# Kernel optimization log

Measured on AMD Instinct MI355X. Metric: run time of the kernel, lower is better.

Reference implementation:

```python
import jax, jax.numpy as jnp
import numpy as np

B, S, D_IN, E, H, WIN = 2, 4096, 512, 512, 8, 128
HD = E // H
NEG = -1e30


def setup_inputs() -> dict:
    key = jax.random.key(0)
    k0, k1, k2 = jax.random.split(key, 3)
    x = jax.random.normal(k0, (B, S, D_IN), jnp.float32)
    w_qkv = jax.random.normal(k1, (D_IN, 3 * E), jnp.float32) / np.sqrt(D_IN)
    b_qkv = jnp.zeros((3 * E,), jnp.float32)
    w_o = jax.random.normal(k2, (E, E), jnp.float32) / np.sqrt(E)
    b_o = jnp.zeros((E,), jnp.float32)
    return dict(x=x, w_qkv=w_qkv, b_qkv=b_qkv, w_o=w_o, b_o=b_o)


def _sliding_window_attn(q, k, v, w):
    # q,k,v: (B, S, H, HD). Longformer sliding-chunks: each query attends to
    # keys within +/- w positions (band of 2w+1), out-of-range masked to -inf.
    b, s, h, hd = q.shape
    assert s % (2 * w) == 0
    c = s // w  # number of width-w query chunks
    qc = q.transpose(0, 2, 1, 3).reshape(b, h, c, w, hd)  # (B,H,C,w,HD)

    def windows(t):
        # build per-chunk 3w key/value windows [c*w - w, c*w + 2w)
        t = t.transpose(0, 2, 1, 3)  # (B,H,S,HD)
        t = jnp.pad(t, ((0, 0), (0, 0), (w, w), (0, 0)))
        t = t.reshape(b, h, c + 2, w, hd)
        return jnp.concatenate([t[:, :, 0:c], t[:, :, 1:c + 1], t[:, :, 2:c + 2]], axis=3)  # (B,H,C,3w,HD)

    kc = windows(k)
    vc = windows(v)

    # chunked logits over the 3w window, scaled by sqrt(d_k)
    logits3 = jnp.einsum('bhcxd,bhcyd->bhcxy', qc, kc) / jnp.sqrt(jnp.asarray(hd, q.dtype))

    # extract diagonal band: band[x, r] = logits3[x, x + r], r in [0, 2w]
    row = jnp.arange(w)[:, None]            # (w,1)
    col = row + jnp.arange(2 * w + 1)[None, :]  # (w,2w+1), index into 3w window
    band = logits3[..., row, col]           # (B,H,C,w,2w+1)

    # mask positions outside [0, S): global key j = i + r - w
    i = (jnp.arange(c) * w)[:, None, None] + jnp.arange(w)[None, :, None]  # (C,w,1)
    j = i + (jnp.arange(2 * w + 1) - w)[None, None, :]                      # (C,w,2w+1)
    valid = (j >= 0) & (j < s)
    band = jnp.where(valid, band, NEG)

    probs = jax.nn.softmax(band, axis=-1)  # (B,H,C,w,2w+1)

    # scatter band probs back into the 3w window and contract with values
    probs3 = jnp.zeros_like(logits3).at[..., row, col].set(probs)  # (B,H,C,w,3w)
    out = jnp.einsum('bhcxy,bhcyd->bhcxd', probs3, vc)  # (B,H,C,w,HD)
    return out.reshape(b, h, s, hd).transpose(0, 2, 1, 3)  # (B,S,H,HD)


def reference(x, w_qkv, b_qkv, w_o, b_o):
    bsz, s, _ = x.shape
    qkv = x @ w_qkv + b_qkv                      # (B,S,3E)
    qkv = qkv.reshape(bsz, s, H, 3 * HD)
    q = qkv[..., :HD]
    k = qkv[..., HD:2 * HD]
    v = qkv[..., 2 * HD:]
    vals = _sliding_window_attn(q, k, v, WIN).reshape(bsz, s, E)
    return vals @ w_o + b_o
```

## Files before the change

kernel.cpp:

```cpp
#include <hip/hip_runtime.h>
#include <hip/hip_bf16.h>
#include <math.h>

typedef _Float16 f16;
typedef __attribute__((ext_vector_type(8))) _Float16 f16x8;
typedef __attribute__((ext_vector_type(4))) _Float16 f16x4;
typedef __attribute__((ext_vector_type(4))) float f32x4;

#define S_LEN 4096
#define NHEAD 8
#define HDIM 64
#define EMB 512
#define KDIM 512
#define LOG2E 1.4426950408889634f

#if __has_builtin(__builtin_amdgcn_exp2f)
#define EXP2F(x) __builtin_amdgcn_exp2f(x)
#else
#define EXP2F(x) exp2f(x)
#endif

__device__ __forceinline__ void g2l16(const void* g, void* l) {
  __builtin_amdgcn_global_load_lds(
      reinterpret_cast<const __attribute__((address_space(1))) unsigned int*>(
          reinterpret_cast<uintptr_t>(g)),
      reinterpret_cast<__attribute__((address_space(3))) unsigned int*>(
          static_cast<unsigned int>(reinterpret_cast<uintptr_t>(l))),
      16, 0, 0);
}

__global__ __launch_bounds__(256) void prep_kernel(
    const float* __restrict__ x, f16* __restrict__ xb,
    const float* __restrict__ w_qkv, f16* __restrict__ wqkvt,
    const float* __restrict__ w_o, f16* __restrict__ wot) {
  __shared__ f16 tile[64][65];
  const int bid = blockIdx.x;
  const int tid = threadIdx.x;
  if (bid < 4096) {
    const int i = (bid * 256 + tid) * 4;
    float4 v = *(const float4*)(x + i);
    f16x4 o = { (f16)v.x, (f16)v.y, (f16)v.z, (f16)v.w };
    *(f16x4*)(xb + i) = o;
    return;
  }
  const float* in;
  f16* out;
  int R, C, c0, r0;
  if (bid < 4288) {
    const int t = bid - 4096;
    in = w_qkv; out = wqkvt; R = 512; C = 1536;
    c0 = (t % 24) * 64; r0 = (t / 24) * 64;
  } else {
    const int t = bid - 4288;
    in = w_o; out = wot; R = 512; C = 512;
    c0 = (t & 7) * 64; r0 = (t >> 3) * 64;
  }
#pragma unroll
  for (int i = 0; i < 16; ++i) {
    const int idx = i * 256 + tid;
    const int lr = idx >> 6, lc = idx & 63;
    tile[lr][lc] = (f16)in[(size_t)(r0 + lr) * C + (c0 + lc)];
  }
  __syncthreads();
#pragma unroll
  for (int i = 0; i < 16; ++i) {
    const int idx = i * 256 + tid;
    const int lc = idx >> 6, lr = idx & 63;
    out[(size_t)(c0 + lc) * R + (r0 + lr)] = tile[lr][lc];
  }
}

#define TM 128
#define TK 32

template<int MODE, int TN>
__global__ __launch_bounds__(256) void gemm_bt_kernel(
    const f16* __restrict__ A, const f16* __restrict__ Bt, const float* __restrict__ bias,
    f16* __restrict__ Qo, f16* __restrict__ Ko, f16* __restrict__ Vo,
    float* __restrict__ Co, int M, int N) {
  constexpr int JN = TN / 32;
  constexpr int BCH = TN / 64;
  constexpr int SMEMSZ = (MODE == 0) ? (128 * 136 * 2) : (8192 + TN * TK * 2);
  __shared__ __align__(16) char smem[SMEMSZ];
  f16 (*As)[TK] = (f16 (*)[TK])smem;
  f16 (*Bs)[TK] = (f16 (*)[TK])(smem + 8192);
  const int m0 = blockIdx.x * TM, n0 = blockIdx.y * TN;
  const int tid = threadIdx.x;
  const int lane = tid & 63, wid = tid >> 6;
  const int wr = wid >> 1, wc = wid & 1;
  const int g = lane >> 4, q16 = lane & 15;

  const int srow = lane >> 2;
  const int skof = (lane & 3) * 8;
  const f16* Ag[2]; char* Al[2];
#pragma unroll
  for (int cb = 0; cb < 2; ++cb) {
    const int ch = wid * 2 + cb;
    Ag[cb] = A + (size_t)(m0 + ch * 16 + srow) * KDIM + skof;
    Al[cb] = (char*)As + ch * 1024;
  }
  const f16* Bg[BCH]; char* Bl[BCH];
#pragma unroll
  for (int cb = 0; cb < BCH; ++cb) {
    const int ch = wid * BCH + cb;
    Bg[cb] = Bt + (size_t)(n0 + ch * 16 + srow) * KDIM + skof;
    Bl[cb] = (char*)Bs + ch * 1024;
  }

  f32x4 zero = {0.f, 0.f, 0.f, 0.f};
  f32x4 acc[4][JN];
#pragma unroll
  for (int i = 0; i < 4; i++)
#pragma unroll
    for (int j = 0; j < JN; j++) acc[i][j] = zero;

  for (int kk = 0; kk < KDIM; kk += TK) {
    g2l16(Ag[0] + kk, Al[0]);
    g2l16(Ag[1] + kk, Al[1]);
#pragma unroll
    for (int cb = 0; cb < BCH; ++cb) g2l16(Bg[cb] + kk, Bl[cb]);
    __syncthreads();
    f16x8 af[4], bfr[JN];
#pragma unroll
    for (int i = 0; i < 4; i++) af[i] = *(const f16x8*)&As[wr * 64 + i * 16 + q16][8 * g];
#pragma unroll
    for (int j = 0; j < JN; j++) bfr[j] = *(const f16x8*)&Bs[wc * (TN / 2) + j * 16 + q16][8 * g];
#pragma unroll
    for (int i = 0; i < 4; i++)
#pragma unroll
      for (int j = 0; j < JN; j++)
        acc[i][j] = __builtin_amdgcn_mfma_f32_16x16x32_f16(af[i], bfr[j], acc[i][j], 0, 0, 0);
    __syncthreads();
  }

  if (MODE == 1) {
#pragma unroll
    for (int i = 0; i < 4; i++)
#pragma unroll
      for (int j = 0; j < JN; j++) {
        const int n = n0 + wc * (TN / 2) + j * 16 + q16;
        const float bs = bias[n];
        const int mbase = m0 + wr * 64 + i * 16 + 4 * g;
#pragma unroll
        for (int r = 0; r < 4; r++) Co[(size_t)(mbase + r) * N + n] = acc[i][j][r] + bs;
      }
  } else {
    f16 (*Cs)[136] = (f16 (*)[136])smem;
#pragma unroll
    for (int i = 0; i < 4; i++)
#pragma unroll
      for (int j = 0; j < JN; j++) {
        const int n = n0 + wc * (TN / 2) + j * 16 + q16;
        const float bs = bias[n];
        const int rr_n = n % 192;
        const float scale = (rr_n < 64) ? 0.125f : 1.0f;
        const int mrow = wr * 64 + i * 16 + 4 * g;
        const int ncol = wc * (TN / 2) + j * 16 + q16;
#pragma unroll
        for (int r = 0; r < 4; r++)
          Cs[mrow + r][ncol] = (f16)((acc[i][j][r] + bs) * scale);
      }
    __syncthreads();
    const int cc = tid & 15;
    const int nn = n0 + 8 * cc;
    const int hh = nn / 192;
    const int rr = nn - 192 * hh;
    f16* base = (rr < 64) ? Qo : (rr < 128) ? Ko : Vo;
    const int d0 = rr & 63;
#pragma unroll
    for (int it = 0; it < 8; ++it) {
      const int m = (tid >> 4) + 16 * it;
      f16x8 v = *(const f16x8*)&Cs[m][8 * cc];
      const int mglob = m0 + m;
      const int b = mglob >> 12, s = mglob & (S_LEN - 1);
      const size_t bh = (size_t)b * NHEAD + hh;
      *(f16x8*)(base + (bh * S_LEN + s) * HDIM + d0) = v;
    }
  }
}

#define VSOFF 49152

__global__ __launch_bounds__(512) void attn_kernel(
    const f16* __restrict__ Q, const f16* __restrict__ K,
    const f16* __restrict__ V, f16* __restrict__ O) {
  __shared__ __align__(16) char smem[98304];

  const int wg = blockIdx.x;
  const int vv = (wg & 7) * 64 + (wg >> 3);
  const int bh = vv >> 5, qc = vv & 31;
  const int b = bh >> 3, h = bh & 7;
  const int tid = threadIdx.x;
  const int wid = tid >> 6, lane = tid & 63;
  const int g = lane >> 4, q16 = lane & 15;
  const int qb = qc * 128;
  const int wb = qb - 128;
  const int qw = qb + wid * 16;
  const int qg = qw + q16;

  const f16* Kb_g = K + (size_t)bh * S_LEN * HDIM;
  const f16* Vb_g = V + (size_t)bh * S_LEN * HDIM;

#pragma unroll
  for (int rd = 0; rd < 6; ++rd) {
    const int idx = rd * 512 + tid;
    const int r = idx >> 3, sl = idx & 7;
    const int key = min(max(wb + r, 0), S_LEN - 1);
    int4 kvv = *(const int4*)(Kb_g + (size_t)key * HDIM + sl * 8);
    *(int4*)(smem + r * 128 + ((sl ^ (r & 7)) << 4)) = kvv;
  }
#pragma unroll
  for (int rd = 0; rd < 6; ++rd) {
    const int idx = rd * 512 + tid;
    const int r = idx >> 3, c8 = (idx & 7) * 8;
    const int key = min(max(wb + r, 0), S_LEN - 1);
    int4 vvv = *(const int4*)(Vb_g + (size_t)key * HDIM + c8);
    *(int4*)(smem + VSOFF + (c8 >> 4) * 12288 + (r >> 2) * 128 + (r & 3) * 32 + ((c8 & 8) << 1)) = vvv;
  }
  __syncthreads();

  const f16* Qb = Q + ((size_t)bh * S_LEN + qw) * HDIM;
  f16x8 qf0 = *(const f16x8*)(Qb + q16 * HDIM + 8 * g);
  f16x8 qf1 = *(const f16x8*)(Qb + q16 * HDIM + 32 + 8 * g);

  f32x4 zero = {0.f, 0.f, 0.f, 0.f};
  f32x4 o[4];
#pragma unroll
  for (int dt = 0; dt < 4; dt++) o[dt] = zero;
  float m_run = 0.f;
  float l_run = 0.f;

  const unsigned troff = (unsigned)(g * 128 + q16 * 8);

#pragma unroll
  for (int t = 0; t < 9; ++t) {
    const int kAp = wid * 16 + 32 * t;
    const int kBp = kAp + 16;
    const int rrA = kAp + q16;
    const int rrB = kBp + q16;
    f16x8 ka0 = *(const f16x8*)(smem + rrA * 128 + (((g    ) ^ (rrA & 7)) << 4));
    f16x8 ka1 = *(const f16x8*)(smem + rrA * 128 + (((g + 4) ^ (rrA & 7)) << 4));
    f16x8 kb0 = *(const f16x8*)(smem + rrB * 128 + (((g    ) ^ (rrB & 7)) << 4));
    f16x8 kb1 = *(const f16x8*)(smem + rrB * 128 + (((g + 4) ^ (rrB & 7)) << 4));

    f32x4 sA = zero, sB = zero;
    __builtin_amdgcn_s_setprio(1);
    sA = __builtin_amdgcn_mfma_f32_16x16x32_f16(ka0, qf0, sA, 0, 0, 0);
    sA = __builtin_amdgcn_mfma_f32_16x16x32_f16(ka1, qf1, sA, 0, 0, 0);
    sB = __builtin_amdgcn_mfma_f32_16x16x32_f16(kb0, qf0, sB, 0, 0, 0);
    sB = __builtin_amdgcn_mfma_f32_16x16x32_f16(kb1, qf1, sB, 0, 0, 0);
    __builtin_amdgcn_s_setprio(0);

    float sv[8];
    float mx = -INFINITY;
#pragma unroll
    for (int i = 0; i < 4; i++) {
      const int kgA = wb + kAp + 4 * g + i;
      const int kgB = wb + kBp + 4 * g + i;
      const bool okA = ((unsigned)(kgA - qg + 128) <= 256u) && ((unsigned)kgA < S_LEN);
      const bool okB = ((unsigned)(kgB - qg + 128) <= 256u) && ((unsigned)kgB < S_LEN);
      sv[i]     = okA ? sA[i] : -INFINITY;
      sv[i + 4] = okB ? sB[i] : -INFINITY;
      mx = fmaxf(mx, fmaxf(sv[i], sv[i + 4]));
    }

    float pA[4], pB[4];
#pragma unroll
    for (int i = 0; i < 4; i++) {
      pA[i] = EXP2F((sv[i] - m_run) * LOG2E);
      pB[i] = EXP2F((sv[i + 4] - m_run) * LOG2E);
    }

    if (__builtin_expect(!__all(mx - m_run <= 8.f), 0)) {
      float mxq = fmaxf(mx, __shfl_xor(mx, 16));
      mxq = fmaxf(mxq, __shfl_xor(mxq, 32));
      const float mnew = fmaxf(m_run, mxq);
      const float resc = EXP2F((m_run - mnew) * LOG2E);
#pragma unroll
      for (int i = 0; i < 4; i++) { pA[i] *= resc; pB[i] *= resc; }
      l_run *= resc;
      float ri[4];
#pragma unroll
      for (int i = 0; i < 4; i++) ri[i] = __shfl(resc, 4 * g + i);
#pragma unroll
      for (int dt = 0; dt < 4; dt++)
#pragma unroll
        for (int i = 0; i < 4; i++) o[dt][i] *= ri[i];
      m_run = mnew;
    }

    f16x4 pfA, pfB;
#pragma unroll
    for (int i = 0; i < 4; i++) {
      l_run += pA[i] + pB[i];
      pfA[i] = (f16)pA[i];
      pfB[i] = (f16)pB[i];
    }

    const int kcA = kAp;
    const int kcB = min(kBp, 368);
    f16x4 bA[4], bB[4];
#pragma unroll
    for (int dt = 0; dt < 4; ++dt) {
      unsigned aA = (unsigned)(uintptr_t)(smem + VSOFF + dt * 12288 + (kcA >> 2) * 128) + troff;
      unsigned aB = (unsigned)(uintptr_t)(smem + VSOFF + dt * 12288 + (kcB >> 2) * 128) + troff;
      asm volatile("ds_read_b64_tr_b16 %0, %1" : "=v"(bA[dt]) : "v"(aA));
      asm volatile("ds_read_b64_tr_b16 %0, %1" : "=v"(bB[dt]) : "v"(aB));
    }
    asm volatile("s_waitcnt lgkmcnt(0)" ::: "memory");
    __builtin_amdgcn_sched_barrier(0);

    __builtin_amdgcn_s_setprio(1);
#pragma unroll
    for (int dt = 0; dt < 4; dt++) {
      o[dt] = __builtin_amdgcn_mfma_f32_16x16x16f16(pfA, bA[dt], o[dt], 0, 0, 0);
      o[dt] = __builtin_amdgcn_mfma_f32_16x16x16f16(pfB, bB[dt], o[dt], 0, 0, 0);
    }
    __builtin_amdgcn_s_setprio(0);
  }

  l_run += __shfl_xor(l_run, 16);
  l_run += __shfl_xor(l_run, 32);
  const float linv = 1.f / l_run;
  float li[4];
#pragma unroll
  for (int i = 0; i < 4; i++) li[i] = __shfl(linv, 4 * g + i);

  __syncthreads();
  float* st = (float*)smem + wid * 1024;
#pragma unroll
  for (int dt = 0; dt < 4; dt++)
#pragma unroll
    for (int i = 0; i < 4; i++)
      st[(4 * g + i) * 64 + dt * 16 + q16] = o[dt][i] * li[i];
  const int r = lane >> 2, c0 = (lane & 3) * 16;
  const float* sp = st + r * 64 + c0;
  f16x8 h0, h1;
#pragma unroll
  for (int j = 0; j < 8; j++) { h0[j] = (f16)sp[j]; h1[j] = (f16)sp[8 + j]; }
  f16* dst = O + ((size_t)b * S_LEN + qw + r) * EMB + h * HDIM + c0;
  *(f16x8*)dst = h0;
  *(f16x8*)(dst + 8) = h1;
}

extern "C" void kernel_launch(void* const* d_in, const int* in_sizes, int n_in,
                              void* d_out, int out_size, void* d_ws, size_t ws_size,
                              hipStream_t stream) {
  const float* x     = (const float*)d_in[0];
  const float* w_qkv = (const float*)d_in[1];
  const float* b_qkv = (const float*)d_in[2];
  const float* w_o   = (const float*)d_in[3];
  const float* b_o   = (const float*)d_in[4];
  float* out = (float*)d_out;

  char* ws = (char*)d_ws;
  f16* xb    = (f16*)(ws);
  f16* wqkvt = (f16*)(ws + 8388608);
  f16* wot   = (f16*)(ws + 9961472);
  f16* Qs    = (f16*)(ws + 10485760);
  f16* Ks    = (f16*)(ws + 18874368);
  f16* Vs    = (f16*)(ws + 27262976);
  f16* attn  = (f16*)(ws + 35651584);

  prep_kernel<<<4352, 256, 0, stream>>>(x, xb, w_qkv, wqkvt, w_o, wot);
  gemm_bt_kernel<0, 128><<<dim3(64, 12), 256, 0, stream>>>(xb, wqkvt, b_qkv, Qs, Ks, Vs,
                                                           (float*)nullptr, 8192, 1536);
  attn_kernel<<<512, 512, 0, stream>>>(Qs, Ks, Vs, attn);
  gemm_bt_kernel<1, 64><<<dim3(64, 8), 256, 0, stream>>>(attn, wot, b_o,
                                                         (f16*)nullptr, (f16*)nullptr, (f16*)nullptr,
                                                         out, 8192, 512);
}
```

Before: 65.71 us.

## Split attention key tiles across two wave groups with flash-style merge

The attention workgroup grows from 512 to 1024 threads. Each query wave is paired with a second wave, and the two split the 9 key tiles between them, 5 and 4. The second group writes its partial output, running max and running sum to shared memory, and the first group rescales and merges them before normalising and storing. The aim is to shorten each wave's serial dependency chain through the window and raise occupancy per CU. The cost is an extra shared-memory merge round, two syncs and a load imbalance between the two halves.

```diff
diff --git a/kernel.cpp b/kernel.cpp
--- a/kernel.cpp
+++ b/kernel.cpp
@@ -181,7 +181,7 @@
 
 #define VSOFF 49152
 
-__global__ __launch_bounds__(512) void attn_kernel(
+__global__ __launch_bounds__(1024) void attn_kernel(
     const f16* __restrict__ Q, const f16* __restrict__ K,
     const f16* __restrict__ V, f16* __restrict__ O) {
   __shared__ __align__(16) char smem[98304];
@@ -192,26 +192,28 @@
   const int b = bh >> 3, h = bh & 7;
   const int tid = threadIdx.x;
   const int wid = tid >> 6, lane = tid & 63;
+  const int qwv = wid & 7;
+  const int kh = wid >> 3;
   const int g = lane >> 4, q16 = lane & 15;
   const int qb = qc * 128;
   const int wb = qb - 128;
-  const int qw = qb + wid * 16;
+  const int qw = qb + qwv * 16;
   const int qg = qw + q16;
 
   const f16* Kb_g = K + (size_t)bh * S_LEN * HDIM;
   const f16* Vb_g = V + (size_t)bh * S_LEN * HDIM;
 
 #pragma unroll
-  for (int rd = 0; rd < 6; ++rd) {
-    const int idx = rd * 512 + tid;
+  for (int rd = 0; rd < 3; ++rd) {
+    const int idx = rd * 1024 + tid;
     const int r = idx >> 3, sl = idx & 7;
     const int key = min(max(wb + r, 0), S_LEN - 1);
     int4 kvv = *(const int4*)(Kb_g + (size_t)key * HDIM + sl * 8);
     *(int4*)(smem + r * 128 + ((sl ^ (r & 7)) << 4)) = kvv;
   }
 #pragma unroll
-  for (int rd = 0; rd < 6; ++rd) {
-    const int idx = rd * 512 + tid;
+  for (int rd = 0; rd < 3; ++rd) {
+    const int idx = rd * 1024 + tid;
     const int r = idx >> 3, c8 = (idx & 7) * 8;
     const int key = min(max(wb + r, 0), S_LEN - 1);
     int4 vvv = *(const int4*)(Vb_g + (size_t)key * HDIM + c8);
@@ -232,9 +234,8 @@
 
   const unsigned troff = (unsigned)(g * 128 + q16 * 8);
 
-#pragma unroll
-  for (int t = 0; t < 9; ++t) {
-    const int kAp = wid * 16 + 32 * t;
+  auto do_tile = [&](int t) {
+    const int kAp = qwv * 16 + 32 * t;
     const int kBp = kAp + 16;
     const int rrA = kAp + q16;
     const int rrB = kBp + q16;
@@ -317,30 +318,64 @@
       o[dt] = __builtin_amdgcn_mfma_f32_16x16x16f16(pfB, bB[dt], o[dt], 0, 0, 0);
     }
     __builtin_amdgcn_s_setprio(0);
+  };
+
+  if (kh == 0) {
+#pragma unroll
+    for (int t = 0; t < 5; ++t) do_tile(t);
+  } else {
+#pragma unroll
+    for (int t = 5; t < 9; ++t) do_tile(t);
   }
 
   l_run += __shfl_xor(l_run, 16);
   l_run += __shfl_xor(l_run, 32);
-  const float linv = 1.f / l_run;
-  float li[4];
-#pragma unroll
-  for (int i = 0; i < 4; i++) li[i] = __shfl(linv, 4 * g + i);
-
+
+  float* oS = (float*)smem;
+  float* lS = (float*)(smem + 32768);
+  float* mS = (float*)(smem + 34816);
   __syncthreads();
-  float* st = (float*)smem + wid * 1024;
-#pragma unroll
-  for (int dt = 0; dt < 4; dt++)
-#pragma unroll
-    for (int i = 0; i < 4; i++)
-      st[(4 * g + i) * 64 + dt * 16 + q16] = o[dt][i] * li[i];
-  const int r = lane >> 2, c0 = (lane & 3) * 16;
-  const float* sp = st + r * 64 + c0;
-  f16x8 h0, h1;
-#pragma unroll
-  for (int j = 0; j < 8; j++) { h0[j] = (f16)sp[j]; h1[j] = (f16)sp[8 + j]; }
-  f16* dst = O + ((size_t)b * S_LEN + qw + r) * EMB + h * HDIM + c0;
-  *(f16x8*)dst = h0;
-  *(f16x8*)(dst + 8) = h1;
+  if (kh == 1) {
+#pragma unroll
+    for (int dt = 0; dt < 4; dt++)
+#pragma unroll
+      for (int i = 0; i < 4; i++)
+        oS[(qwv * 64 + lane) * 16 + dt * 4 + i] = o[dt][i];
+    lS[qwv * 64 + lane] = l_run;
+    mS[qwv * 64 + lane] = m_run;
+  }
+  __syncthreads();
+  if (kh == 0) {
+    const float mB = mS[qwv * 64 + lane];
+    const float lB = lS[qwv * 64 + lane];
+    const float m = fmaxf(m_run, mB);
+    const float fA = EXP2F((m_run - m) * LOG2E);
+    const float fB = EXP2F((mB - m) * LOG2E);
+    const float linv = 1.f / (l_run * fA + lB * fB);
+    const float aA = fA * linv, aB = fB * linv;
+    float aAi[4], aBi[4];
+#pragma unroll
+    for (int i = 0; i < 4; i++) {
+      aAi[i] = __shfl(aA, 4 * g + i);
+      aBi[i] = __shfl(aB, 4 * g + i);
+    }
+    float* st = (float*)(smem + VSOFF) + qwv * 1024;
+#pragma unroll
+    for (int dt = 0; dt < 4; dt++)
+#pragma unroll
+      for (int i = 0; i < 4; i++) {
+        const float ov = o[dt][i] * aAi[i] + oS[(qwv * 64 + lane) * 16 + dt * 4 + i] * aBi[i];
+        st[(4 * g + i) * 64 + dt * 16 + q16] = ov;
+      }
+    const int r = lane >> 2, c0 = (lane & 3) * 16;
+    const float* sp = st + r * 64 + c0;
+    f16x8 h0, h1;
+#pragma unroll
+    for (int j = 0; j < 8; j++) { h0[j] = (f16)sp[j]; h1[j] = (f16)sp[8 + j]; }
+    f16* dst = O + ((size_t)b * S_LEN + qw + r) * EMB + h * HDIM + c0;
+    *(f16x8*)dst = h0;
+    *(f16x8*)(dst + 8) = h1;
+  }
 }
 
 extern "C" void kernel_launch(void* const* d_in, const int* in_sizes, int n_in,
@@ -365,7 +400,7 @@
   prep_kernel<<<4352, 256, 0, stream>>>(x, xb, w_qkv, wqkvt, w_o, wot);
   gemm_bt_kernel<0, 128><<<dim3(64, 12), 256, 0, stream>>>(xb, wqkvt, b_qkv, Qs, Ks, Vs,
                                                            (float*)nullptr, 8192, 1536);
-  attn_kernel<<<512, 512, 0, stream>>>(Qs, Ks, Vs, attn);
+  attn_kernel<<<512, 1024, 0, stream>>>(Qs, Ks, Vs, attn);
   gemm_bt_kernel<1, 64><<<dim3(64, 8), 256, 0, stream>>>(attn, wot, b_o,
                                                          (f16*)nullptr, (f16*)nullptr, (f16*)nullptr,
                                                          out, 8192, 512);
```

Result: no change. 65.36 us (-0.5%).
